# Kernel tuning notes

Hardware: AMD Instinct MI355X
Metric: run time of the kernel (lower is better)

## Reference

```python
import jax, jax.numpy as jnp
import numpy as np

N_POINTS = 100000
N_EVENTS = 1000000
N_PAIRS = 100000      # node_pair_samples
N_RIEMANN = 128       # riemann_samples
INIT_BETA = 0.025
NON_EVENT_W = 1.0
EPS = 1e-6            # torch PairwiseDistance default eps (added to the difference)


def setup_inputs() -> dict:
    key = jax.random.key(0)
    ks = jax.random.split(key, 8)
    # learned parameters
    beta = jnp.full((1, 1), INIT_BETA, jnp.float32)
    z0 = jax.random.uniform(ks[0], (N_POINTS, 2), jnp.float32, -0.025, 0.025)
    v0 = jax.random.uniform(ks[1], (N_POINTS, 2), jnp.float32, -0.025, 0.025)
    a0 = jnp.zeros((N_POINTS, 2), jnp.float32)  # a0 is referenced by step(); zero -> constant-velocity
    # event data: (u, v, event_time)
    u = jax.random.randint(ks[2], (N_EVENTS,), 0, N_POINTS)
    v = jax.random.randint(ks[3], (N_EVENTS,), 0, N_POINTS)
    event_times = jax.random.uniform(ks[4], (N_EVENTS,), jnp.float32, 0.0, 1.0)
    # sampled non-event node pairs (stand-in for randperm over triu indices)
    pair_u = jax.random.randint(ks[5], (N_PAIRS,), 0, N_POINTS)
    pair_v = jax.random.randint(ks[6], (N_PAIRS,), 0, N_POINTS)
    pair_v = jnp.where(pair_v == pair_u, (pair_v + 1) % N_POINTS, pair_v)
    t0 = jnp.float32(0.0)
    tn = jnp.float32(1.0)
    return {"beta": beta, "z0": z0, "v0": v0, "a0": a0,
            "u": u, "v": v, "event_times": event_times,
            "pair_u": pair_u, "pair_v": pair_v, "t0": t0, "tn": tn}


def reference(beta, z0, v0, a0, u, v, event_times, pair_u, pair_v, t0, tn):
    b = beta[0, 0]
    # ---- event intensity: sum_e (beta - ||z_u(t_e) - z_v(t_e)||) ----
    te = event_times[:, None]                                  # [E,1]
    zu = z0[u] + v0[u] * te + 0.5 * a0[u] * te ** 2            # [E,2]
    zv = z0[v] + v0[v] * te + 0.5 * a0[v] * te ** 2            # [E,2]
    d_ev = jnp.sqrt(jnp.sum((zu - zv + EPS) ** 2, axis=-1))    # [E]
    event_intensity = b * event_times.shape[0] - jnp.sum(d_ev)
    # ---- non-event intensity: Riemann sum of exp(beta - d(t)) over sampled pairs ----
    ts = t0 + (jnp.arange(N_RIEMANN, dtype=jnp.float32) / N_RIEMANN) * (tn - t0)  # [T] left Riemann
    dt = (tn - t0) / N_RIEMANN
    dz = z0[pair_u] - z0[pair_v]                               # [P,2]
    dv = v0[pair_u] - v0[pair_v]
    da = a0[pair_u] - a0[pair_v]
    tt = ts[None, :, None]                                     # [1,T,1]
    diff = dz[:, None, :] + dv[:, None, :] * tt + 0.5 * da[:, None, :] * tt ** 2 + EPS  # [P,T,2]
    d_ne = jnp.sqrt(jnp.sum(diff ** 2, axis=-1))               # [P,T]
    non_event_intensity = jnp.sum(jnp.exp(b - d_ne)) * dt
    return event_intensity - NON_EVENT_W * non_event_intensity
```

## Files before the change

kernel.cpp:

```cpp
#include <hip/hip_runtime.h>
#include <hip/hip_fp16.h>

#define N_POINTS   100000
#define N_EVENTS   1000000
#define N_PAIRS    100000
#define N_RIEMANN  128
#define EPS_F      1e-6f
#define NON_EVENT_W 1.0f

constexpr int BLOCK       = 256;
constexpr int EVPT        = 8;
constexpr int EV_THREADS  = N_EVENTS / EVPT;
constexpr int EV_BLOCKS   = (EV_THREADS + BLOCK - 1) / BLOCK;
constexpr int PAIR_BLOCKS = (N_PAIRS + BLOCK - 1) / BLOCK;
constexpr int MAIN_BLOCKS = PAIR_BLOCKS + EV_BLOCKS;
constexpr int PREP_BLOCKS = (N_POINTS + BLOCK - 1) / BLOCK;


__device__ __forceinline__ float block_reduce_sum(float v) {
    #pragma unroll
    for (int off = 32; off > 0; off >>= 1)
        v += __shfl_down(v, off, 64);
    __shared__ float smem[BLOCK / 64];
    const int lane = threadIdx.x & 63;
    const int wid  = threadIdx.x >> 6;
    if (lane == 0) smem[wid] = v;
    __syncthreads();
    float r = 0.f;
    if (threadIdx.x == 0) {
        #pragma unroll
        for (int i = 0; i < BLOCK / 64; ++i) r += smem[i];
    }
    return r;
}

__device__ __forceinline__ void decode_rec(const float4& r, float2& z, float2& v, float2& a) {
    z = __half22float2(*reinterpret_cast<const __half2*>(&r.x));
    v = __half22float2(*reinterpret_cast<const __half2*>(&r.y));
    a = __half22float2(*reinterpret_cast<const __half2*>(&r.z));
}

__global__ __launch_bounds__(BLOCK) void prep_kernel(
    const float2* __restrict__ z0,
    const float2* __restrict__ v0,
    const float2* __restrict__ a0,
    float4*       __restrict__ pts)
{
    const int i = blockIdx.x * BLOCK + threadIdx.x;
    if (i < N_POINTS) {
        const float2 z = z0[i], v = v0[i], a = a0[i];
        float4 r;
        *reinterpret_cast<__half2*>(&r.x) = __float22half2_rn(make_float2(z.x, z.y));
        *reinterpret_cast<__half2*>(&r.y) = __float22half2_rn(make_float2(v.x, v.y));
        *reinterpret_cast<__half2*>(&r.z) = __float22half2_rn(make_float2(a.x, a.y));
        r.w = 0.f;
        pts[i] = r;
    }
}

template <bool PACKED>
__global__ __launch_bounds__(BLOCK) void main_kernel(
    const float4* __restrict__ pts,
    const float2* __restrict__ z0,
    const float2* __restrict__ v0,
    const float2* __restrict__ a0,
    const float*  __restrict__ beta,
    const int*    __restrict__ eu,
    const int*    __restrict__ ev,
    const float*  __restrict__ et,
    const int*    __restrict__ pu,
    const int*    __restrict__ pv,
    const float*  __restrict__ t0p,
    const float*  __restrict__ tnp,
    float*        __restrict__ partials)
{
    float acc = 0.f;
    const int b = blockIdx.x;

    if (b < PAIR_BLOCKS) {
        const int p = b * BLOCK + threadIdx.x;
        if (p < N_PAIRS) {
            const float t0v = t0p[0];
            const float tnv = tnp[0];
            const float dt  = (tnv - t0v) * (1.0f / N_RIEMANN);
            const float bb  = beta[0];
            const int iu = pu[p];
            const int iv = pv[p];
            float dzx, dzy, dvx, dvy, dax, day;
            if (PACKED) {
                const float4 ru = pts[iu];
                const float4 rv = pts[iv];
                float2 zu, vu, au, zv, vv, av;
                decode_rec(ru, zu, vu, au);
                decode_rec(rv, zv, vv, av);
                dzx = zu.x - zv.x; dzy = zu.y - zv.y;
                dvx = vu.x - vv.x; dvy = vu.y - vv.y;
                dax = au.x - av.x; day = au.y - av.y;
            } else {
                const float2 zu = z0[iu], zv = z0[iv];
                const float2 vu = v0[iu], vv = v0[iv];
                const float2 au = a0[iu], av = a0[iv];
                dzx = zu.x - zv.x; dzy = zu.y - zv.y;
                dvx = vu.x - vv.x; dvy = vu.y - vv.y;
                dax = au.x - av.x; day = au.y - av.y;
            }
            const float eb = __expf(bb);
            float s = 0.f;
            #pragma unroll 4
            for (int k = 0; k < N_RIEMANN; ++k) {
                const float t = t0v + (float)k * (1.0f / N_RIEMANN) * (tnv - t0v);
                const float h = 0.5f * t * t;
                const float dx = dzx + dvx * t + dax * h + EPS_F;
                const float dy = dzy + dvy * t + day * h + EPS_F;
                s += __expf(-sqrtf(dx * dx + dy * dy));
            }
            acc = -NON_EVENT_W * dt * eb * s;
        }
    } else {
        const int t = (b - PAIR_BLOCKS) * BLOCK + threadIdx.x;
        if (t < EV_THREADS) {
            const int4*   eu4 = reinterpret_cast<const int4*>(eu);
            const int4*   ev4 = reinterpret_cast<const int4*>(ev);
            const float4* et4 = reinterpret_cast<const float4*>(et);
            const int4 u0 = eu4[2 * t], u1 = eu4[2 * t + 1];
            const int4 w0 = ev4[2 * t], w1 = ev4[2 * t + 1];
            const float4 t0q = et4[2 * t], t1q = et4[2 * t + 1];
            const int iu[EVPT] = { u0.x, u0.y, u0.z, u0.w, u1.x, u1.y, u1.z, u1.w };
            const int iv[EVPT] = { w0.x, w0.y, w0.z, w0.w, w1.x, w1.y, w1.z, w1.w };
            const float te[EVPT] = { t0q.x, t0q.y, t0q.z, t0q.w, t1q.x, t1q.y, t1q.z, t1q.w };
            if (PACKED) {
                float4 ru[EVPT], rv[EVPT];
                #pragma unroll
                for (int j = 0; j < EVPT; ++j) ru[j] = pts[iu[j]];
                #pragma unroll
                for (int j = 0; j < EVPT; ++j) rv[j] = pts[iv[j]];
                #pragma unroll
                for (int j = 0; j < EVPT; ++j) {
                    float2 zu, vu, au, zv, vv, av;
                    decode_rec(ru[j], zu, vu, au);
                    decode_rec(rv[j], zv, vv, av);
                    const float h = 0.5f * te[j] * te[j];
                    const float dx = (zu.x - zv.x) + (vu.x - vv.x) * te[j] + (au.x - av.x) * h + EPS_F;
                    const float dy = (zu.y - zv.y) + (vu.y - vv.y) * te[j] + (au.y - av.y) * h + EPS_F;
                    acc -= sqrtf(dx * dx + dy * dy);
                }
            } else {
                #pragma unroll
                for (int j = 0; j < EVPT; ++j) {
                    const float2 zu = z0[iu[j]], zv = z0[iv[j]];
                    const float2 vu = v0[iu[j]], vv = v0[iv[j]];
                    const float2 au = a0[iu[j]], av = a0[iv[j]];
                    const float h = 0.5f * te[j] * te[j];
                    const float dx = (zu.x - zv.x) + (vu.x - vv.x) * te[j] + (au.x - av.x) * h + EPS_F;
                    const float dy = (zu.y - zv.y) + (vu.y - vv.y) * te[j] + (au.y - av.y) * h + EPS_F;
                    acc -= sqrtf(dx * dx + dy * dy);
                }
            }
        }
    }

    const float r = block_reduce_sum(acc);
    if (threadIdx.x == 0) partials[blockIdx.x] = r;
}

__global__ __launch_bounds__(BLOCK) void reduce_kernel(
    const float* __restrict__ partials,
    const float* __restrict__ beta,
    float*       __restrict__ out)
{
    float acc = 0.f;
    for (int i = threadIdx.x; i < MAIN_BLOCKS; i += BLOCK) acc += partials[i];
    const float r = block_reduce_sum(acc);
    if (threadIdx.x == 0) out[0] = beta[0] * (float)N_EVENTS + r;
}

extern "C" void kernel_launch(void* const* d_in, const int* in_sizes, int n_in,
                              void* d_out, int out_size, void* d_ws, size_t ws_size,
                              hipStream_t stream) {
    const float*  beta = (const float*)d_in[0];
    const float2* z0   = (const float2*)d_in[1];
    const float2* v0   = (const float2*)d_in[2];
    const float2* a0   = (const float2*)d_in[3];
    const int*    eu   = (const int*)d_in[4];
    const int*    ev   = (const int*)d_in[5];
    const float*  et   = (const float*)d_in[6];
    const int*    pu   = (const int*)d_in[7];
    const int*    pv   = (const int*)d_in[8];
    const float*  t0p  = (const float*)d_in[9];
    const float*  tnp  = (const float*)d_in[10];

    float* out = (float*)d_out;
    const size_t pts_bytes = (size_t)N_POINTS * sizeof(float4);
    const bool packed = (ws_size >= pts_bytes + (size_t)MAIN_BLOCKS * sizeof(float));

    if (packed) {
        float4* pts      = (float4*)d_ws;
        float*  partials = (float*)((char*)d_ws + pts_bytes);
        prep_kernel<<<PREP_BLOCKS, BLOCK, 0, stream>>>(z0, v0, a0, pts);
        main_kernel<true><<<MAIN_BLOCKS, BLOCK, 0, stream>>>(
            pts, z0, v0, a0, beta, eu, ev, et, pu, pv, t0p, tnp, partials);
        reduce_kernel<<<1, BLOCK, 0, stream>>>(partials, beta, out);
    } else {
        float* partials = (float*)d_ws;
        main_kernel<false><<<MAIN_BLOCKS, BLOCK, 0, stream>>>(
            nullptr, z0, v0, a0, beta, eu, ev, et, pu, pv, t0p, tnp, partials);
        reduce_kernel<<<1, BLOCK, 0, stream>>>(partials, beta, out);
    }
}
```

Before: 105.3 us.

## Split Riemann steps across two threads per pair and fuse final reduction via atomics

Each sampled pair is now handled by two threads, each summing half of the Riemann steps, which doubles pair-side parallelism and shortens the longest per-thread loop. The separate reduce kernel is removed: each block atomically adds its partial into the output, which is zeroed with a memset, and the beta*N_EVENTS term is added by one block. Launch bounds now request four blocks per SM. This trades one kernel launch for a memset plus about 4k float atomics, and the floating-point summation order becomes nondeterministic.

After: 108.6 us. 1.03x slower.

```diff
diff --git a/kernel.cpp b/kernel.cpp
--- a/kernel.cpp
+++ b/kernel.cpp
@@ -12,9 +12,12 @@
 constexpr int EVPT        = 8;
 constexpr int EV_THREADS  = N_EVENTS / EVPT;
 constexpr int EV_BLOCKS   = (EV_THREADS + BLOCK - 1) / BLOCK;
-constexpr int PAIR_BLOCKS = (N_PAIRS + BLOCK - 1) / BLOCK;
+constexpr int PAIR_SPLIT  = 2;
+constexpr int PAIR_THREADS= N_PAIRS * PAIR_SPLIT;
+constexpr int PAIR_BLOCKS = (PAIR_THREADS + BLOCK - 1) / BLOCK;
 constexpr int MAIN_BLOCKS = PAIR_BLOCKS + EV_BLOCKS;
 constexpr int PREP_BLOCKS = (N_POINTS + BLOCK - 1) / BLOCK;
+constexpr int STEPS_PER   = N_RIEMANN / PAIR_SPLIT;
 
 
 __device__ __forceinline__ float block_reduce_sum(float v) {
@@ -59,7 +62,7 @@
 }
 
 template <bool PACKED>
-__global__ __launch_bounds__(BLOCK) void main_kernel(
+__global__ __launch_bounds__(BLOCK, 4) void main_kernel(
     const float4* __restrict__ pts,
     const float2* __restrict__ z0,
     const float2* __restrict__ v0,
@@ -72,14 +75,16 @@
     const int*    __restrict__ pv,
     const float*  __restrict__ t0p,
     const float*  __restrict__ tnp,
-    float*        __restrict__ partials)
+    float*        __restrict__ out)
 {
     float acc = 0.f;
     const int b = blockIdx.x;
 
     if (b < PAIR_BLOCKS) {
-        const int p = b * BLOCK + threadIdx.x;
-        if (p < N_PAIRS) {
+        const int idx = b * BLOCK + threadIdx.x;
+        if (idx < PAIR_THREADS) {
+            const int p    = idx >> 1;
+            const int half = idx & 1;
             const float t0v = t0p[0];
             const float tnv = tnp[0];
             const float dt  = (tnv - t0v) * (1.0f / N_RIEMANN);
@@ -105,9 +110,10 @@
                 dax = au.x - av.x; day = au.y - av.y;
             }
             const float eb = __expf(bb);
+            const int k0 = half * STEPS_PER;
             float s = 0.f;
             #pragma unroll 4
-            for (int k = 0; k < N_RIEMANN; ++k) {
+            for (int k = k0; k < k0 + STEPS_PER; ++k) {
                 const float t = t0v + (float)k * (1.0f / N_RIEMANN) * (tnv - t0v);
                 const float h = 0.5f * t * t;
                 const float dx = dzx + dvx * t + dax * h + EPS_F;
@@ -157,21 +163,12 @@
                 }
             }
         }
+        if (b == PAIR_BLOCKS && threadIdx.x == 0)
+            acc += beta[0] * (float)N_EVENTS;
     }
 
     const float r = block_reduce_sum(acc);
-    if (threadIdx.x == 0) partials[blockIdx.x] = r;
-}
-
-__global__ __launch_bounds__(BLOCK) void reduce_kernel(
-    const float* __restrict__ partials,
-    const float* __restrict__ beta,
-    float*       __restrict__ out)
-{
-    float acc = 0.f;
-    for (int i = threadIdx.x; i < MAIN_BLOCKS; i += BLOCK) acc += partials[i];
-    const float r = block_reduce_sum(acc);
-    if (threadIdx.x == 0) out[0] = beta[0] * (float)N_EVENTS + r;
+    if (threadIdx.x == 0) atomicAdd(out, r);
 }
 
 extern "C" void kernel_launch(void* const* d_in, const int* in_sizes, int n_in,
@@ -191,19 +188,17 @@
 
     float* out = (float*)d_out;
     const size_t pts_bytes = (size_t)N_POINTS * sizeof(float4);
-    const bool packed = (ws_size >= pts_bytes + (size_t)MAIN_BLOCKS * sizeof(float));
+    const bool packed = (ws_size >= pts_bytes);
+
+    hipMemsetAsync(out, 0, sizeof(float), stream);
 
     if (packed) {
-        float4* pts      = (float4*)d_ws;
-        float*  partials = (float*)((char*)d_ws + pts_bytes);
+        float4* pts = (float4*)d_ws;
         prep_kernel<<<PREP_BLOCKS, BLOCK, 0, stream>>>(z0, v0, a0, pts);
         main_kernel<true><<<MAIN_BLOCKS, BLOCK, 0, stream>>>(
-            pts, z0, v0, a0, beta, eu, ev, et, pu, pv, t0p, tnp, partials);
-        reduce_kernel<<<1, BLOCK, 0, stream>>>(partials, beta, out);
+            pts, z0, v0, a0, beta, eu, ev, et, pu, pv, t0p, tnp, out);
     } else {
-        float* partials = (float*)d_ws;
         main_kernel<false><<<MAIN_BLOCKS, BLOCK, 0, stream>>>(
-            nullptr, z0, v0, a0, beta, eu, ev, et, pu, pv, t0p, tnp, partials);
-        reduce_kernel<<<1, BLOCK, 0, stream>>>(partials, beta, out);
-    }
-}
+            nullptr, z0, v0, a0, beta, eu, ev, et, pu, pv, t0p, tnp, out);
+    }
+}
```
